# Optimization experiments

Measured on AMD Instinct MI355X. Metric: run time of the kernel, lower is better.

Reference implementation:

```python
import jax, jax.numpy as jnp
import numpy as np

TEMP1 = 4.0  # local_temp1 default


def setup_inputs() -> dict:
    key = jax.random.key(0)
    k1, k2 = jax.random.split(key)
    query = jax.random.normal(k1, (256, 768, 96), dtype=jnp.float32)
    context = jax.random.normal(k2, (256, 768, 19, 19), dtype=jnp.float32)
    return {"query": query, "context": context}


def reference(query, context):
    # query: [B, ndf, Q]; context: [B, ndf, ih, iw]
    B, ndf, Q = query.shape
    ih, iw = context.shape[2], context.shape[3]
    S = ih * iw
    ctx = context.reshape(B, ndf, S)            # [B, ndf, S]
    # attn = contextT @ query -> [B, S, Q]
    attn = jnp.einsum('bds,bdq->bsq', ctx, query)
    # softmax over query dim
    attn = jax.nn.softmax(attn, axis=-1)
    # transpose to [B, Q, S], temperature scale, softmax over source dim
    attn = jnp.swapaxes(attn, 1, 2) * TEMP1
    attn = jax.nn.softmax(attn, axis=-1)        # [B, Q, S]
    # weightedContext = context @ attn^T -> [B, ndf, Q]
    weighted_context = jnp.einsum('bds,bqs->bdq', ctx, attn)
    attn_map = attn.reshape(B, Q, ih, iw)
    return weighted_context, attn_map
```

## Files before the change

### kernel.cpp

```cpp
#include <hip/hip_runtime.h>

#define NB 256
#define NDF 768
#define NQ 96
#define NS 361
#define LDT 40
#define LDP 392
#define WSROW 368
#define WS_LOG_BYTES ((size_t)NB * NQ * WSROW * 2)

typedef short bf16x8_t __attribute__((ext_vector_type(8)));
typedef float f32x4_t __attribute__((ext_vector_type(4)));
typedef float f32x4u_t __attribute__((ext_vector_type(4), aligned(4)));
typedef unsigned int u32x4_t __attribute__((ext_vector_type(4)));

__device__ __forceinline__ unsigned pack_hi(unsigned b_, unsigned a_) {
    return __builtin_amdgcn_perm(b_, a_, 0x07060302u);
}
__device__ __forceinline__ unsigned short f2bf(float x) {
    unsigned u = __float_as_uint(x);
    u += 0x7FFFu + ((u >> 16) & 1u);
    return (unsigned short)(u >> 16);
}
__device__ __forceinline__ float bf2f(unsigned short h) {
    return __uint_as_float(((unsigned)h) << 16);
}

__device__ __forceinline__ void cvt8(const float* x, bf16x8_t& hi, bf16x8_t& lo) {
    unsigned uh[8]; float fl[8];
#pragma unroll
    for (int j = 0; j < 8; ++j) {
        unsigned u = __float_as_uint(x[j]);
        uh[j] = u;
        fl[j] = x[j] - __uint_as_float(u & 0xFFFF0000u);
    }
    u32x4_t h, l;
    h[0] = pack_hi(uh[1], uh[0]); h[1] = pack_hi(uh[3], uh[2]);
    h[2] = pack_hi(uh[5], uh[4]); h[3] = pack_hi(uh[7], uh[6]);
    l[0] = pack_hi(__float_as_uint(fl[1]), __float_as_uint(fl[0]));
    l[1] = pack_hi(__float_as_uint(fl[3]), __float_as_uint(fl[2]));
    l[2] = pack_hi(__float_as_uint(fl[5]), __float_as_uint(fl[4]));
    l[3] = pack_hi(__float_as_uint(fl[7]), __float_as_uint(fl[6]));
    hi = __builtin_bit_cast(bf16x8_t, h);
    lo = __builtin_bit_cast(bf16x8_t, l);
}

__device__ __forceinline__ void block_sync_lds() {
    asm volatile("s_waitcnt lgkmcnt(0)" ::: "memory");
    __builtin_amdgcn_s_barrier();
    __builtin_amdgcn_sched_barrier(0);
}

#define GLD(D, A)     asm volatile("global_load_dword %0, %1, off" : "=v"(D) : "v"(A))
#define GLDO(D, A, O) asm volatile("global_load_dword %0, %1, off offset:" #O : "=v"(D) : "v"(A))
#define VMWAIT(N) { asm volatile("s_waitcnt vmcnt(" #N ")"); __builtin_amdgcn_sched_barrier(0); }

template<int MODE>
__global__ __launch_bounds__(384, 3) void k1_gemm1_softmaxq(
    const float* __restrict__ Qg, const float* __restrict__ Cg,
    unsigned short* __restrict__ WsLog, float* __restrict__ AoutF)
{
    __shared__ __align__(16) unsigned short sQhi[2][NQ * LDT];
    __shared__ __align__(16) unsigned short sQlo[2][NQ * LDT];

    const int x = blockIdx.x;
    const int b = (x & 7) * 32 + (x >> 4);
    const int h = (x >> 3) & 1;

    const int tid = threadIdx.x;
    const int wv = tid >> 6;
    const int lane = tid & 63;
    const int ll = lane & 15;
    const int lg = lane >> 4;
    const int llh = (ll >> 3) & 1;
    const int s0 = 192 * h;
    const int qq = tid % 96;
    const int koct = tid / 96;
    const int sc0 = min(s0 + 32 * wv + ll, NS - 1);
    const int sc1 = min(s0 + 32 * wv + 16 + ll, NS - 1);
    const int stoff = qq * LDT + 8 * (koct ^ ((qq >> 3) & 3));

    const float* __restrict__ qg = Qg + (size_t)b * NDF * NQ;
    const float* __restrict__ cg = Cg + (size_t)b * NDF * NS;

    f32x4_t acc[6][2];
#pragma unroll
    for (int i = 0; i < 6; ++i)
#pragma unroll
        for (int j = 0; j < 2; ++j) acc[i][j] = (f32x4_t)0.0f;

    float qv[8], cA[16], cB[16];

#define ISSUE_Q(K0) { \
    unsigned long long qa = (unsigned long long)(qg + ((K0) + 8 * koct) * NQ + qq); \
    GLD (qv[0], qa);        GLDO(qv[1], qa, 384); \
    GLDO(qv[2], qa, 768);   GLDO(qv[3], qa, 1152); \
    GLDO(qv[4], qa, 1536);  GLDO(qv[5], qa, 1920); \
    GLDO(qv[6], qa, 2304);  GLDO(qv[7], qa, 2688); }

#define ISSUE_CTX(K0, R) { \
    unsigned long long p0 = (unsigned long long)(cg + (size_t)((K0) + 8 * lg) * NS + sc0); \
    unsigned long long p1 = p0 + 3u * NS * 4u; \
    unsigned long long p2 = p0 + 6u * NS * 4u; \
    GLD (R[0], p0); GLDO(R[1], p0, 1444); GLDO(R[2], p0, 2888); \
    GLD (R[3], p1); GLDO(R[4], p1, 1444); GLDO(R[5], p1, 2888); \
    GLD (R[6], p2); GLDO(R[7], p2, 1444); \
    unsigned long long p3 = (unsigned long long)(cg + (size_t)((K0) + 8 * lg) * NS + sc1); \
    unsigned long long p4 = p3 + 3u * NS * 4u; \
    unsigned long long p5 = p3 + 6u * NS * 4u; \
    GLD (R[8],  p3); GLDO(R[9],  p3, 1444); GLDO(R[10], p3, 2888); \
    GLD (R[11], p4); GLDO(R[12], p4, 1444); GLDO(R[13], p4, 2888); \
    GLD (R[14], p5); GLDO(R[15], p5, 1444); }

#define STAGEQ(CUR) { \
    bf16x8_t qh, ql; \
    cvt8(qv, qh, ql); \
    *(bf16x8_t*)&sQhi[CUR][stoff] = qh; \
    *(bf16x8_t*)&sQlo[CUR][stoff] = ql; }

#define MFMAPH(R, CUR) { \
    bf16x8_t B0h, B0l, B1h, B1l; \
    cvt8(R, B0h, B0l); \
    cvt8(R + 8, B1h, B1l); \
    _Pragma("unroll") \
    for (int mt = 0; mt < 6; ++mt) { \
        int ro = (16 * mt + ll) * LDT + 8 * (lg ^ ((2 * mt + llh) & 3)); \
        bf16x8_t Ah = *(const bf16x8_t*)&sQhi[CUR][ro]; \
        bf16x8_t Al = *(const bf16x8_t*)&sQlo[CUR][ro]; \
        acc[mt][0] = __builtin_amdgcn_mfma_f32_16x16x32_bf16(Ah, B0h, acc[mt][0], 0, 0, 0); \
        acc[mt][0] = __builtin_amdgcn_mfma_f32_16x16x32_bf16(Ah, B0l, acc[mt][0], 0, 0, 0); \
        acc[mt][0] = __builtin_amdgcn_mfma_f32_16x16x32_bf16(Al, B0h, acc[mt][0], 0, 0, 0); \
        acc[mt][1] = __builtin_amdgcn_mfma_f32_16x16x32_bf16(Ah, B1h, acc[mt][1], 0, 0, 0); \
        acc[mt][1] = __builtin_amdgcn_mfma_f32_16x16x32_bf16(Ah, B1l, acc[mt][1], 0, 0, 0); \
        acc[mt][1] = __builtin_amdgcn_mfma_f32_16x16x32_bf16(Al, B1h, acc[mt][1], 0, 0, 0); } }

#define ITER(C, USE, FILL, CUR, NXT) { \
    ISSUE_Q(((C) + 1) * 32); \
    ISSUE_CTX(((C) + 1) * 32, FILL); \
    VMWAIT(24); \
    MFMAPH(USE, CUR); \
    VMWAIT(16); \
    STAGEQ(NXT); \
    block_sync_lds(); }

    ISSUE_Q(0);
    ISSUE_CTX(0, cA);
    VMWAIT(16);
    STAGEQ(0);
    block_sync_lds();

    for (int c = 0; c < 22; c += 2) {
        ITER(c,     cA, cB, 0, 1);
        ITER(c + 1, cB, cA, 1, 0);
    }
    ITER(22, cA, cB, 0, 1);
    VMWAIT(0);
    MFMAPH(cB, 1);

#undef ISSUE_Q
#undef ISSUE_CTX
#undef STAGEQ
#undef MFMAPH
#undef ITER

#pragma unroll
    for (int nt = 0; nt < 2; ++nt) {
        float m = -3.0e38f;
#pragma unroll
        for (int mt = 0; mt < 6; ++mt)
#pragma unroll
            for (int r = 0; r < 4; ++r) m = fmaxf(m, acc[mt][nt][r]);
        m = fmaxf(m, __shfl_xor(m, 16));
        m = fmaxf(m, __shfl_xor(m, 32));
        float sum = 0.0f;
#pragma unroll
        for (int mt = 0; mt < 6; ++mt)
#pragma unroll
            for (int r = 0; r < 4; ++r) {
                float e = __expf(acc[mt][nt][r] - m);
                acc[mt][nt][r] = e;
                sum += e;
            }
        sum += __shfl_xor(sum, 16);
        sum += __shfl_xor(sum, 32);
        float inv = 4.0f / sum;
#pragma unroll
        for (int mt = 0; mt < 6; ++mt)
#pragma unroll
            for (int r = 0; r < 4; ++r) acc[mt][nt][r] *= inv;
    }

    if constexpr (MODE >= 1) {
        unsigned short* wr = WsLog + (size_t)b * NQ * WSROW;
#pragma unroll
        for (int mt = 0; mt < 6; ++mt)
#pragma unroll
            for (int nt = 0; nt < 2; ++nt)
#pragma unroll
                for (int r = 0; r < 4; ++r) {
                    int q = 16 * mt + 4 * lg + r;
                    int s = s0 + 32 * wv + 16 * nt + ll;
                    if (s < NS) wr[q * WSROW + s] = f2bf(acc[mt][nt][r]);
                }
    } else {
        float* aout = AoutF + (size_t)b * NQ * NS;
#pragma unroll
        for (int mt = 0; mt < 6; ++mt)
#pragma unroll
            for (int nt = 0; nt < 2; ++nt)
#pragma unroll
                for (int r = 0; r < 4; ++r) {
                    int q = 16 * mt + 4 * lg + r;
                    int s = s0 + 32 * wv + 16 * nt + ll;
                    if (s < NS) aout[(size_t)q * NS + s] = acc[mt][nt][r];
                }
    }
}

__global__ __launch_bounds__(256) void k15_softmaxs(float* __restrict__ Aout)
{
    const int b = blockIdx.x;
    const int q = blockIdx.y * 4 + (threadIdx.x >> 6);
    const int lane = threadIdx.x & 63;
    float* __restrict__ row = Aout + ((size_t)b * NQ + q) * NS;
    const int c0 = 6 * lane;

    float v[6];
#pragma unroll
    for (int i = 0; i < 6; ++i) v[i] = (c0 + i < NS) ? row[c0 + i] : -INFINITY;
    float m = v[0];
#pragma unroll
    for (int i = 1; i < 6; ++i) m = fmaxf(m, v[i]);
#pragma unroll
    for (int o = 1; o < 64; o <<= 1) m = fmaxf(m, __shfl_xor(m, o));
    float e[6], sum = 0.0f;
#pragma unroll
    for (int i = 0; i < 6; ++i) { e[i] = __expf(v[i] - m); sum += e[i]; }
#pragma unroll
    for (int o = 1; o < 64; o <<= 1) sum += __shfl_xor(sum, o);
    float inv = 1.0f / sum;
#pragma unroll
    for (int i = 0; i < 6; ++i) if (c0 + i < NS) row[c0 + i] = e[i] * inv;
}

template<bool FUSED>
__global__ __launch_bounds__(512, 4) void k2_gemm2(
    const float* __restrict__ Cg, const unsigned short* __restrict__ WsLog,
    const float* __restrict__ AttnF, float* __restrict__ Wout, float* __restrict__ AoutF)
{
    extern __shared__ char smem2[];
    unsigned short* sP = (unsigned short*)smem2;
    unsigned* sPd = (unsigned*)smem2;
    float* sMax = (float*)(smem2 + NQ * LDP * 2);
    float* sInv = sMax + NQ;

    const int x = blockIdx.x;
    const int b = (x & 7) * 32 + (x >> 5);
    const int quarter = (x >> 3) & 3;
    const int tid = threadIdx.x;
    const int wv = tid >> 6;
    const int lane = tid & 63;
    const int ll = lane & 15;
    const int lg = lane >> 4;

    if constexpr (FUSED) {
        const unsigned* __restrict__ wsd = (const unsigned*)(WsLog + (size_t)b * NQ * WSROW);
        for (int i = tid; i < NQ * 184; i += 512) {
            int r = i / 184, c = i - r * 184;
            sPd[r * 196 + c] = wsd[i];
        }
        for (int i = tid; i < NQ * 12; i += 512) {
            int r = i / 12, c = i - r * 12;
            sPd[r * 196 + 184 + c] = 0;
        }
        __syncthreads();

        const int l32 = tid & 31;
        const int rbase = tid >> 5;
#pragma unroll
        for (int pass = 0; pass < 6; ++pass) {
            int row = pass * 16 + rbase;
            float m = -3.0e38f;
#pragma unroll
            for (int j = 0; j < 6; ++j) {
                int dw = l32 + 32 * j;
                if (dw < 184) {
                    unsigned u = sPd[row * 196 + dw];
                    float v0 = bf2f((unsigned short)(u & 0xFFFFu));
                    float v1 = bf2f((unsigned short)(u >> 16));
                    if (2 * dw < NS) m = fmaxf(m, v0);
                    if (2 * dw + 1 < NS) m = fmaxf(m, v1);
                }
            }
#pragma unroll
            for (int o = 1; o < 32; o <<= 1) m = fmaxf(m, __shfl_xor(m, o));
            if (l32 == 0) sMax[row] = m;
        }
        __syncthreads();
#pragma unroll
        for (int pass = 0; pass < 6; ++pass) {
            int row = pass * 16 + rbase;
            float m = sMax[row];
            float sum = 0.0f;
#pragma unroll
            for (int j = 0; j < 6; ++j) {
                int dw = l32 + 32 * j;
                if (dw < 184) {
                    unsigned u = sPd[row * 196 + dw];
                    float v0 = bf2f((unsigned short)(u & 0xFFFFu));
                    float v1 = bf2f((unsigned short)(u >> 16));
                    float e0 = (2 * dw < NS) ? __expf(v0 - m) : 0.0f;
                    float e1 = (2 * dw + 1 < NS) ? __expf(v1 - m) : 0.0f;
                    sum += e0 + e1;
                    sPd[row * 196 + dw] = ((unsigned)f2bf(e1) << 16) | (unsigned)f2bf(e0);
                }
            }
#pragma unroll
            for (int o = 1; o < 32; o <<= 1) sum += __shfl_xor(sum, o);
            if (l32 == 0) sInv[row] = sum;
        }
        __syncthreads();
        if (tid < NQ) sInv[tid] = 1.0f / sInv[tid];
        __syncthreads();
        if (quarter == 0) {
            float* aout = AoutF + (size_t)b * NQ * NS;
            for (int i = tid; i < NQ * NS; i += 512) {
                int q = i / NS, s = i - q * NS;
                aout[i] = bf2f(sP[q * LDP + s]) * sInv[q];
            }
        }
    } else {
        const float* __restrict__ attn = AttnF + (size_t)b * NQ * NS;
        for (int i = tid; i < NQ * 181; i += 512) {
            int row = i / 181, p = i - row * 181;
            float x0 = attn[row * NS + 2 * p];
            float x1 = (p < 180) ? attn[row * NS + 2 * p + 1] : 0.0f;
            sPd[row * 196 + p] = pack_hi(__float_as_uint(x1), __float_as_uint(x0));
        }
        for (int i = tid; i < NQ * 15; i += 512) {
            int row = i / 15, p = i - row * 15;
            sPd[row * 196 + 181 + p] = 0;
        }
        __syncthreads();
    }

    f32x4_t acc[3][3];
#pragma unroll
    for (int i = 0; i < 3; ++i)
#pragma unroll
        for (int j = 0; j < 3; ++j) acc[i][j] = (f32x4_t)0.0f;

    const int dw = wv >> 1, qw = wv & 1;
    const float* __restrict__ cq = Cg + (size_t)b * NDF * NS + (size_t)(quarter * 192) * NS;

#pragma unroll
    for (int c = 0; c < 12; ++c) {
        bf16x8_t Bf[3];
#pragma unroll
        for (int nt = 0; nt < 3; ++nt) {
            int row = 16 * (3 * qw + nt) + ll;
            Bf[nt] = *(const bf16x8_t*)&sP[row * LDP + 32 * c + 8 * lg];
        }
#pragma unroll
        for (int i = 0; i < 3; ++i) {
            int d = 16 * (3 * dw + i) + ll;
            const float* ap = cq + (size_t)d * NS + 32 * c + 8 * lg;
            u32x4_t u;
            if (c < 11) {
                f32x4u_t a0 = *(const f32x4u_t*)ap;
                f32x4u_t a1 = *(const f32x4u_t*)(ap + 4);
                u[0] = pack_hi(__float_as_uint(a0[1]), __float_as_uint(a0[0]));
                u[1] = pack_hi(__float_as_uint(a0[3]), __float_as_uint(a0[2]));
                u[2] = pack_hi(__float_as_uint(a1[1]), __float_as_uint(a1[0]));
                u[3] = pack_hi(__float_as_uint(a1[3]), __float_as_uint(a1[2]));
            } else {
                float t[8];
#pragma unroll
                for (int e = 0; e < 8; ++e) {
                    int s = 352 + 8 * lg + e;
                    t[e] = (s < NS) ? ap[e] : 0.0f;
                }
                u[0] = pack_hi(__float_as_uint(t[1]), __float_as_uint(t[0]));
                u[1] = pack_hi(__float_as_uint(t[3]), __float_as_uint(t[2]));
                u[2] = pack_hi(__float_as_uint(t[5]), __float_as_uint(t[4]));
                u[3] = pack_hi(__float_as_uint(t[7]), __float_as_uint(t[6]));
            }
            bf16x8_t Af = __builtin_bit_cast(bf16x8_t, u);
#pragma unroll
            for (int nt = 0; nt < 3; ++nt)
                acc[i][nt] = __builtin_amdgcn_mfma_f32_16x16x32_bf16(Af, Bf[nt], acc[i][nt], 0, 0, 0);
        }
    }

    float* wout = Wout + (size_t)b * NDF * NQ;
    float invq[3];
#pragma unroll
    for (int nt = 0; nt < 3; ++nt) {
        if constexpr (FUSED) invq[nt] = sInv[16 * (3 * qw + nt) + ll];
        else invq[nt] = 1.0f;
    }
#pragma unroll
    for (int i = 0; i < 3; ++i)
#pragma unroll
        for (int nt = 0; nt < 3; ++nt)
#pragma unroll
            for (int r = 0; r < 4; ++r) {
                int d = quarter * 192 + 16 * (3 * dw + i) + 4 * lg + r;
                int q = 16 * (3 * qw + nt) + ll;
                wout[(size_t)d * NQ + q] = acc[i][nt][r] * invq[nt];
            }
}

extern "C" void kernel_launch(void* const* d_in, const int* in_sizes, int n_in,
                              void* d_out, int out_size, void* d_ws, size_t ws_size,
                              hipStream_t stream) {
    const float* Qg = (const float*)d_in[0];
    const float* Cg = (const float*)d_in[1];
    float* Wout = (float*)d_out;
    float* Aout = Wout + (size_t)NB * NDF * NQ;

    const int smem2 = NQ * LDP * 2 + NQ * 8;

    if (ws_size >= WS_LOG_BYTES) {
        unsigned short* wsLog = (unsigned short*)d_ws;
        k1_gemm1_softmaxq<1><<<dim3(NB * 2), dim3(384), 0, stream>>>(Qg, Cg, wsLog, nullptr);
        (void)hipFuncSetAttribute((const void*)k2_gemm2<true>,
                                  hipFuncAttributeMaxDynamicSharedMemorySize, smem2);
        k2_gemm2<true><<<dim3(NB * 4), dim3(512), smem2, stream>>>(
            Cg, wsLog, nullptr, Wout, Aout);
    } else {
        k1_gemm1_softmaxq<0><<<dim3(NB * 2), dim3(384), 0, stream>>>(Qg, Cg, nullptr, Aout);
        k15_softmaxs<<<dim3(NB, 24), dim3(256), 0, stream>>>(Aout);
        (void)hipFuncSetAttribute((const void*)k2_gemm2<false>,
                                  hipFuncAttributeMaxDynamicSharedMemorySize, smem2);
        k2_gemm2<false><<<dim3(NB * 4), dim3(512), smem2, stream>>>(
            Cg, nullptr, Aout, Wout, Aout);
    }
}
```

Baseline: 206.8 us.

## Load context as dwordx2 pairs and deepen global-load pipeline to two stages

Result: slower. 212.0 us (+2.5%).

```diff
diff --git a/kernel.cpp b/kernel.cpp
--- a/kernel.cpp
+++ b/kernel.cpp
@@ -10,6 +10,7 @@
 #define WS_LOG_BYTES ((size_t)NB * NQ * WSROW * 2)
 
 typedef short bf16x8_t __attribute__((ext_vector_type(8)));
+typedef float f32x2_t __attribute__((ext_vector_type(2)));
 typedef float f32x4_t __attribute__((ext_vector_type(4)));
 typedef float f32x4u_t __attribute__((ext_vector_type(4), aligned(4)));
 typedef unsigned int u32x4_t __attribute__((ext_vector_type(4)));
@@ -51,8 +52,10 @@
     __builtin_amdgcn_sched_barrier(0);
 }
 
-#define GLD(D, A)     asm volatile("global_load_dword %0, %1, off" : "=v"(D) : "v"(A))
-#define GLDO(D, A, O) asm volatile("global_load_dword %0, %1, off offset:" #O : "=v"(D) : "v"(A))
+#define GLD(D, A)       asm volatile("global_load_dword %0, %1, off" : "=v"(D) : "v"(A))
+#define GLDO(D, A, O)   asm volatile("global_load_dword %0, %1, off offset:" #O : "=v"(D) : "v"(A))
+#define GLD2(D, A)      asm volatile("global_load_dwordx2 %0, %1, off" : "=v"(D) : "v"(A))
+#define GLD2O(D, A, O)  asm volatile("global_load_dwordx2 %0, %1, off offset:" #O : "=v"(D) : "v"(A))
 #define VMWAIT(N) { asm volatile("s_waitcnt vmcnt(" #N ")"); __builtin_amdgcn_sched_barrier(0); }
 
 template<int MODE>
@@ -76,12 +79,14 @@
     const int s0 = 192 * h;
     const int qq = tid % 96;
     const int koct = tid / 96;
-    const int sc0 = min(s0 + 32 * wv + ll, NS - 1);
-    const int sc1 = min(s0 + 32 * wv + 16 + ll, NS - 1);
+    const int spRaw = s0 + 32 * wv + 2 * ll;
+    const int sp0c  = min(spRaw, NS - 2);
+    const bool bsel = (spRaw > NS - 2);
     const int stoff = qq * LDT + 8 * (koct ^ ((qq >> 3) & 3));
 
     const float* __restrict__ qg = Qg + (size_t)b * NDF * NQ;
     const float* __restrict__ cg = Cg + (size_t)b * NDF * NS;
+    const float* __restrict__ cgl = cg + sp0c;
 
     f32x4_t acc[6][2];
 #pragma unroll
@@ -89,39 +94,39 @@
 #pragma unroll
         for (int j = 0; j < 2; ++j) acc[i][j] = (f32x4_t)0.0f;
 
-    float qv[8], cA[16], cB[16];
-
-#define ISSUE_Q(K0) { \
+    float qv0[8], qv1[8];
+    f32x2_t rcA[8], rcB[8], rcC[8];
+
+#define ISSUE_Q(K0, QV) { \
     unsigned long long qa = (unsigned long long)(qg + ((K0) + 8 * koct) * NQ + qq); \
-    GLD (qv[0], qa);        GLDO(qv[1], qa, 384); \
-    GLDO(qv[2], qa, 768);   GLDO(qv[3], qa, 1152); \
-    GLDO(qv[4], qa, 1536);  GLDO(qv[5], qa, 1920); \
-    GLDO(qv[6], qa, 2304);  GLDO(qv[7], qa, 2688); }
+    GLD (QV[0], qa);        GLDO(QV[1], qa, 384); \
+    GLDO(QV[2], qa, 768);   GLDO(QV[3], qa, 1152); \
+    GLDO(QV[4], qa, 1536);  GLDO(QV[5], qa, 1920); \
+    GLDO(QV[6], qa, 2304);  GLDO(QV[7], qa, 2688); }
 
 #define ISSUE_CTX(K0, R) { \
-    unsigned long long p0 = (unsigned long long)(cg + (size_t)((K0) + 8 * lg) * NS + sc0); \
-    unsigned long long p1 = p0 + 3u * NS * 4u; \
-    unsigned long long p2 = p0 + 6u * NS * 4u; \
-    GLD (R[0], p0); GLDO(R[1], p0, 1444); GLDO(R[2], p0, 2888); \
-    GLD (R[3], p1); GLDO(R[4], p1, 1444); GLDO(R[5], p1, 2888); \
-    GLD (R[6], p2); GLDO(R[7], p2, 1444); \
-    unsigned long long p3 = (unsigned long long)(cg + (size_t)((K0) + 8 * lg) * NS + sc1); \
-    unsigned long long p4 = p3 + 3u * NS * 4u; \
-    unsigned long long p5 = p3 + 6u * NS * 4u; \
-    GLD (R[8],  p3); GLDO(R[9],  p3, 1444); GLDO(R[10], p3, 2888); \
-    GLD (R[11], p4); GLDO(R[12], p4, 1444); GLDO(R[13], p4, 2888); \
-    GLD (R[14], p5); GLDO(R[15], p5, 1444); }
-
-#define STAGEQ(CUR) { \
+    unsigned long long p0 = (unsigned long long)(cgl + (size_t)((K0) + 8 * lg) * NS); \
+    unsigned long long p1 = p0 + 3u * 1444u; \
+    unsigned long long p2 = p0 + 6u * 1444u; \
+    GLD2 (R[0], p0); GLD2O(R[1], p0, 1444); GLD2O(R[2], p0, 2888); \
+    GLD2 (R[3], p1); GLD2O(R[4], p1, 1444); GLD2O(R[5], p1, 2888); \
+    GLD2 (R[6], p2); GLD2O(R[7], p2, 1444); }
+
+#define STAGEQ(QV, CUR) { \
     bf16x8_t qh, ql; \
-    cvt8(qv, qh, ql); \
+    cvt8(QV, qh, ql); \
     *(bf16x8_t*)&sQhi[CUR][stoff] = qh; \
     *(bf16x8_t*)&sQlo[CUR][stoff] = ql; }
 
 #define MFMAPH(R, CUR) { \
+    float xe[8], xo[8]; \
+    _Pragma("unroll") \
+    for (int j = 0; j < 8; ++j) { \
+        xe[j] = bsel ? R[j][1] : R[j][0]; \
+        xo[j] = R[j][1]; } \
     bf16x8_t B0h, B0l, B1h, B1l; \
-    cvt8(R, B0h, B0l); \
-    cvt8(R + 8, B1h, B1l); \
+    cvt8(xe, B0h, B0l); \
+    cvt8(xo, B1h, B1l); \
     _Pragma("unroll") \
     for (int mt = 0; mt < 6; ++mt) { \
         int ro = (16 * mt + ll) * LDT + 8 * (lg ^ ((2 * mt + llh) & 3)); \
@@ -134,28 +139,40 @@
         acc[mt][1] = __builtin_amdgcn_mfma_f32_16x16x32_bf16(Ah, B1l, acc[mt][1], 0, 0, 0); \
         acc[mt][1] = __builtin_amdgcn_mfma_f32_16x16x32_bf16(Al, B1h, acc[mt][1], 0, 0, 0); } }
 
-#define ITER(C, USE, FILL, CUR, NXT) { \
-    ISSUE_Q(((C) + 1) * 32); \
-    ISSUE_CTX(((C) + 1) * 32, FILL); \
+#define ITER(C, USE, FILL, QISS, QSTG, CUR, NXT) { \
+    ISSUE_Q(((C) + 2) * 32, QISS); \
+    ISSUE_CTX(((C) + 2) * 32, FILL); \
+    VMWAIT(32); \
+    MFMAPH(USE, CUR); \
     VMWAIT(24); \
-    MFMAPH(USE, CUR); \
-    VMWAIT(16); \
-    STAGEQ(NXT); \
+    STAGEQ(QSTG, NXT); \
     block_sync_lds(); }
 
-    ISSUE_Q(0);
-    ISSUE_CTX(0, cA);
+    ISSUE_Q(0, qv0);   ISSUE_CTX(0, rcA);
+    ISSUE_Q(32, qv1);  ISSUE_CTX(32, rcB);
+    VMWAIT(24);
+    STAGEQ(qv0, 0);
+    block_sync_lds();
+
+    for (int cc = 0; cc < 18; cc += 6) {
+        ITER(cc + 0, rcA, rcC, qv0, qv1, 0, 1);
+        ITER(cc + 1, rcB, rcA, qv1, qv0, 1, 0);
+        ITER(cc + 2, rcC, rcB, qv0, qv1, 0, 1);
+        ITER(cc + 3, rcA, rcC, qv1, qv0, 1, 0);
+        ITER(cc + 4, rcB, rcA, qv0, qv1, 0, 1);
+        ITER(cc + 5, rcC, rcB, qv1, qv0, 1, 0);
+    }
+    ITER(18, rcA, rcC, qv0, qv1, 0, 1);
+    ITER(19, rcB, rcA, qv1, qv0, 1, 0);
+    ITER(20, rcC, rcB, qv0, qv1, 0, 1);
+    ITER(21, rcA, rcC, qv1, qv0, 1, 0);
     VMWAIT(16);
-    STAGEQ(0);
+    MFMAPH(rcB, 0);
+    VMWAIT(8);
+    STAGEQ(qv1, 1);
     block_sync_lds();
-
-    for (int c = 0; c < 22; c += 2) {
-        ITER(c,     cA, cB, 0, 1);
-        ITER(c + 1, cB, cA, 1, 0);
-    }
-    ITER(22, cA, cB, 0, 1);
     VMWAIT(0);
-    MFMAPH(cB, 1);
+    MFMAPH(rcC, 1);
 
 #undef ISSUE_Q
 #undef ISSUE_CTX
@@ -199,7 +216,7 @@
 #pragma unroll
                 for (int r = 0; r < 4; ++r) {
                     int q = 16 * mt + 4 * lg + r;
-                    int s = s0 + 32 * wv + 16 * nt + ll;
+                    int s = s0 + 32 * wv + 2 * ll + nt;
                     if (s < NS) wr[q * WSROW + s] = f2bf(acc[mt][nt][r]);
                 }
     } else {
@@ -211,7 +228,7 @@
 #pragma unroll
                 for (int r = 0; r < 4; ++r) {
                     int q = 16 * mt + 4 * lg + r;
-                    int s = s0 + 32 * wv + 16 * nt + ll;
+                    int s = s0 + 32 * wv + 2 * ll + nt;
                     if (s < NS) aout[(size_t)q * NS + s] = acc[mt][nt][r];
                 }
     }
```
